# Optimization experiments

Measured on AMD Instinct MI355X. Metric: run time of the kernel, lower is better.

## Reference

```python
import jax, jax.numpy as jnp
import numpy as np

GRID_SIZE = 5
SPLINE_ORDER = 3
GRID_LO, GRID_HI = -1.0, 1.0


def _make_grid():
    # extended knot vector: grid_size + 2*spline_order intervals
    h = (GRID_HI - GRID_LO) / GRID_SIZE
    return jnp.arange(-SPLINE_ORDER, GRID_SIZE + SPLINE_ORDER + 1, dtype=jnp.float32) * h + GRID_LO


def _b_splines(x, grid):
    # x: [N, F] -> bases [N, F, GRID_SIZE + SPLINE_ORDER] via Cox-de Boor recursion
    xg = x[..., None]
    bases = ((xg >= grid[:-1]) & (xg < grid[1:])).astype(x.dtype)
    for k in range(1, SPLINE_ORDER + 1):
        left = (xg - grid[: -(k + 1)]) / (grid[k:-1] - grid[: -(k + 1)])
        right = (grid[k + 1:] - xg) / (grid[k + 1:] - grid[1:-k])
        bases = left * bases[..., :-1] + right * bases[..., 1:]
    return bases


def _kan_linear(x, base_w, spline_w, spline_scaler, grid):
    # x: [N, in], base_w: [out, in], spline_w: [out, in, K], spline_scaler: [out, in]
    base_out = jax.nn.relu(x) @ base_w.T
    n = x.shape[0]
    sw = (spline_w * spline_scaler[..., None]).reshape(base_w.shape[0], -1)  # [out, in*K]
    spline_out = _b_splines(x, grid).reshape(n, -1) @ sw.T
    return base_out + spline_out


def _kan_conv(x, base_w, spline_w, spline_scaler, grid, k=5):
    # x: [B, C, H, W] -> KANLinear over unfolded 5x5 patches (stride 1, VALID)
    B, C, H, W = x.shape
    patches = jax.lax.conv_general_dilated_patches(x, (k, k), (1, 1), 'VALID')  # [B, C*k*k, Ho, Wo]
    Ho, Wo = patches.shape[2], patches.shape[3]
    p = patches.transpose(0, 2, 3, 1).reshape(B * Ho * Wo, C * k * k)
    out = _kan_linear(p, base_w, spline_w, spline_scaler, grid)
    return out.reshape(B, Ho, Wo, -1).transpose(0, 3, 1, 2)


def _avgpool2(x):
    B, C, H, W = x.shape
    return x.reshape(B, C, H // 2, 2, W // 2, 2).mean(axis=(3, 5))


def setup_inputs() -> dict:
    key = jax.random.key(0)
    ks = jax.random.split(key, 13)
    s = 0.1
    return {
        'x': jax.random.normal(ks[0], (1024, 1, 28, 28), jnp.float32),
        'c1_base_w': jax.random.normal(ks[1], (6, 25), jnp.float32) * s,
        'c1_spline_w': jax.random.normal(ks[2], (6, 25, 8), jnp.float32) * s,
        'c1_spline_scaler': jax.random.normal(ks[3], (6, 25), jnp.float32) * s,
        'c2_base_w': jax.random.normal(ks[4], (16, 150), jnp.float32) * s,
        'c2_spline_w': jax.random.normal(ks[5], (16, 150, 8), jnp.float32) * s,
        'c2_spline_scaler': jax.random.normal(ks[6], (16, 150), jnp.float32) * s,
        'fc1_w': jax.random.normal(ks[7], (120, 256), jnp.float32) * s,
        'fc1_b': jax.random.normal(ks[8], (120,), jnp.float32) * s,
        'fc2_w': jax.random.normal(ks[9], (84, 120), jnp.float32) * s,
        'fc2_b': jax.random.normal(ks[10], (84,), jnp.float32) * s,
        'fc3_w': jax.random.normal(ks[11], (62, 84), jnp.float32) * s,
        'fc3_b': jax.random.normal(ks[12], (62,), jnp.float32) * s,
    }


def reference(x, c1_base_w, c1_spline_w, c1_spline_scaler,
              c2_base_w, c2_spline_w, c2_spline_scaler,
              fc1_w, fc1_b, fc2_w, fc2_b, fc3_w, fc3_b):
    grid = _make_grid()
    h = _kan_conv(x, c1_base_w, c1_spline_w, c1_spline_scaler, grid)   # [B,6,24,24]
    h = _avgpool2(h)                                                    # [B,6,12,12]
    h = _kan_conv(h, c2_base_w, c2_spline_w, c2_spline_scaler, grid)   # [B,16,8,8]
    h = _avgpool2(h)                                                    # [B,16,4,4]
    h = h.reshape(h.shape[0], -1)                                       # [B,256]
    h = jax.nn.relu(h @ fc1_w.T + fc1_b)
    h = jax.nn.relu(h @ fc2_w.T + fc2_b)
    return h @ fc3_w.T + fc3_b                                          # [B,62]
```

## Files before the change

### kernel.cpp

```cpp
#include <hip/hip_runtime.h>


typedef _Float16 f16;
typedef f16 f16x8 __attribute__((ext_vector_type(8)));
typedef float f32x4 __attribute__((ext_vector_type(4)));

#define ONE_SIXTH 0.16666666666666666f

__device__ __forceinline__ void spline9(float v, float* __restrict__ f) {
    float u  = 2.5f * v + 5.5f;
    bool valid = (u >= 0.0f) && (u < 11.0f);
    float fi = floorf(u);
    int   i  = (int)fi;
    float w  = u - fi;
    float omw = 1.0f - w;
    float w2 = w * w, w3 = w2 * w;
    float c0 = omw * omw * omw * ONE_SIXTH;
    float c1 = (3.0f * w3 - 6.0f * w2 + 4.0f) * ONE_SIXTH;
    float c2 = (-3.0f * w3 + 3.0f * w2 + 3.0f * w + 1.0f) * ONE_SIXTH;
    float c3 = w3 * ONE_SIXTH;
    int j0 = i - 3;
#pragma unroll
    for (int j = 0; j < 8; ++j) {
        int d = j - j0;
        float val = (d == 0) ? c0 : (d == 1) ? c1 : (d == 2) ? c2 : (d == 3) ? c3 : 0.0f;
        f[j] = valid ? val : 0.0f;
    }
    f[8] = fmaxf(v, 0.0f);
}

__device__ __forceinline__ void spline_chunks(float v, uint4& u0, uint4& u1) {
    float f[9];
    spline9(v, f);
    union { f16 h[8]; uint4 u; } a, b;
#pragma unroll
    for (int j = 0; j < 8; ++j) a.h[j] = (f16)f[j];
    b.u.x = 0u; b.u.y = 0u; b.u.z = 0u; b.u.w = 0u;
    b.h[0] = (f16)f[8];
    u0 = a.u; u1 = b.u;
}

__global__ __launch_bounds__(256) void k_prep(
    const float* __restrict__ c1_bw, const float* __restrict__ c1_sw,
    const float* __restrict__ c1_sc,
    const float* __restrict__ c2_bw, const float* __restrict__ c2_sw,
    const float* __restrict__ c2_sc,
    f16* __restrict__ W1g, f16* __restrict__ W2g)
{
    int t = blockIdx.x * 256 + threadIdx.x;
    if (t < 9216) {
        int tap = t >> 8, r = t & 255;
        int o = r >> 4, k = r & 15;
        float val = 0.0f;
        if (o < 6 && k < 9) {
            int ey = tap / 6, ex = tap - 6 * ey;
            float s = 0.0f;
            for (int a = 0; a < 2; ++a) {
                for (int b = 0; b < 2; ++b) {
                    int dy = ey - a, dx = ex - b;
                    if (dy >= 0 && dy < 5 && dx >= 0 && dx < 5) {
                        int idx = o * 25 + dy * 5 + dx;
                        s += (k == 8) ? c1_bw[idx] : c1_sw[idx * 8 + k] * c1_sc[idx];
                    }
                }
            }
            val = 0.25f * s;
        }
        W1g[t] = (f16)val;
    }
    if (t < 55296) {
        int c = t / 9216, r = t - c * 9216;
        int tap = r >> 8, rr = r & 255;
        int o = rr >> 4, k = rr & 15;
        float val = 0.0f;
        if (k < 9) {
            int ey = tap / 6, ex = tap - 6 * ey;
            float s = 0.0f;
            for (int a = 0; a < 2; ++a) {
                for (int b = 0; b < 2; ++b) {
                    int dy = ey - a, dx = ex - b;
                    if (dy >= 0 && dy < 5 && dx >= 0 && dx < 5) {
                        int idx = o * 150 + c * 25 + dy * 5 + dx;
                        s += (k == 8) ? c2_bw[idx] : c2_sw[idx * 8 + k] * c2_sc[idx];
                    }
                }
            }
            val = 0.25f * s;
        }
        W2g[t] = (f16)val;
    }
}

__global__ __launch_bounds__(192, 3) void k_conv12(
    const float* __restrict__ x, const f16* __restrict__ W1g,
    const f16* __restrict__ W2g, float* __restrict__ h2)
{
    __shared__ uint4  feat[1728];
    __shared__ float  h1l[864];
    __shared__ float4 rbuf[2][64];

    const int img = blockIdx.x;
    const int tid = threadIdx.x;
    const int lane = tid & 63, wv = tid >> 6;
    const int ln15 = lane & 15, g = lane >> 4;
    const int gh = g & 1, gt = g >> 1;

    for (int e = tid; e < 784; e += 192) {
        uint4 u0, u1;
        spline_chunks(x[img * 784 + e], u0, u1);
        int ch = e * 2;
        int q = (ch >> 3) & 7;
        feat[ch ^ q] = u0;
        feat[(ch + 1) ^ q] = u1;
    }
    __syncthreads();

    {
        int ebase[3];
#pragma unroll
        for (int t = 0; t < 3; ++t) {
            int p = (wv * 3 + t) * 16 + ln15;
            int py = p / 12, px = p - py * 12;
            ebase[t] = py * 56 + px * 2;
        }
        const f16* bptr = W1g + (gt * 16 + ln15) * 16 + gh * 8;
        f16x8 bfrag = *(const f16x8*)bptr;
        f32x4 acc[3] = {{0,0,0,0},{0,0,0,0},{0,0,0,0}};

        for (int kc = 0; kc < 18; ++kc) {
            int tap = kc * 2 + gt;
            int ey = (tap * 171) >> 10, ex = tap - ey * 6;
            int eoff = ey * 28 + ex;
            f16x8 bcur = bfrag;
            bptr += 512;
            bfrag = *(const f16x8*)bptr;
#pragma unroll
            for (int t = 0; t < 3; ++t) {
                int ch = (ebase[t] + eoff) * 2 + gh;
                ch ^= (ch >> 3) & 7;
                f16x8 afrag = *(const f16x8*)(&feat[ch]);
                acc[t] = __builtin_amdgcn_mfma_f32_16x16x32_f16(afrag, bcur, acc[t], 0, 0, 0);
            }
        }
        if (ln15 < 6) {
#pragma unroll
            for (int t = 0; t < 3; ++t) {
                int p0 = (wv * 3 + t) * 16 + g * 4;
                *(float4*)&h1l[ln15 * 144 + p0] =
                    make_float4(acc[t][0], acc[t][1], acc[t][2], acc[t][3]);
            }
        }
    }
    __syncthreads();

    for (int e = tid; e < 864; e += 192) {
        uint4 u0, u1;
        spline_chunks(h1l[e], u0, u1);
        int ch = e * 2;
        int q = (ch >> 3) & 7;
        feat[ch ^ q] = u0;
        feat[(ch + 1) ^ q] = u1;
    }
    __syncthreads();

    {
        const int py = ln15 >> 2, px = ln15 & 3;
        const int epx = py * 24 + px * 2;
        const int kk0 = wv * 36;
        const f16* bptr = W2g + ((kk0 * 2 + gt) * 16 + ln15) * 16 + gh * 8;
        f16x8 bfrag = *(const f16x8*)bptr;
        f32x4 acc = {0, 0, 0, 0};

        for (int i = 0; i < 36; ++i) {
            int kk = kk0 + i;
            int c = kk / 18, tk = kk - c * 18;
            int tap = tk * 2 + gt;
            int ey = (tap * 171) >> 10, ex = tap - ey * 6;
            f16x8 bcur = bfrag;
            bptr += 512;
            bfrag = *(const f16x8*)bptr;
            int elem = c * 144 + epx + ey * 12 + ex;
            int ch = elem * 2 + gh;
            ch ^= (ch >> 3) & 7;
            f16x8 afrag = *(const f16x8*)(&feat[ch]);
            acc = __builtin_amdgcn_mfma_f32_16x16x32_f16(afrag, bcur, acc, 0, 0, 0);
        }

        if (wv) rbuf[wv - 1][lane] = make_float4(acc[0], acc[1], acc[2], acc[3]);
        __syncthreads();
        if (wv == 0) {
            float4 r0 = rbuf[0][lane], r1 = rbuf[1][lane];
            *(float4*)&h2[img * 256 + ln15 * 16 + g * 4] =
                make_float4(acc[0] + r0.x + r1.x, acc[1] + r0.y + r1.y,
                            acc[2] + r0.z + r1.z, acc[3] + r0.w + r1.w);
        }
    }
}

__global__ __launch_bounds__(256) void k_fc(
    const float* __restrict__ h2,
    const float* __restrict__ w1, const float* __restrict__ b1,
    const float* __restrict__ w2, const float* __restrict__ b2,
    const float* __restrict__ w3, const float* __restrict__ b3,
    float* __restrict__ out)
{
    __shared__ float xin[8][260];
    __shared__ float a1[8][120];
    __shared__ float a2[8][84];
    const int tid = threadIdx.x;
    const int r0 = blockIdx.x * 8;

    for (int i = tid; i < 2048; i += 256)
        xin[i >> 8][i & 255] = h2[r0 * 256 + i];
    __syncthreads();

    for (int idx = tid; idx < 960; idx += 256) {
        const int o = idx >> 3, r = idx & 7;
        const float* w = w1 + o * 256;
        float s = 0.0f;
#pragma unroll 8
        for (int k = 0; k < 64; ++k) {
            float4 wv = ((const float4*)w)[k];
            float4 xv = *(const float4*)(&xin[r][k * 4]);
            s += wv.x * xv.x + wv.y * xv.y + wv.z * xv.z + wv.w * xv.w;
        }
        a1[r][o] = fmaxf(s + b1[o], 0.0f);
    }
    __syncthreads();

    for (int idx = tid; idx < 672; idx += 256) {
        const int o = idx >> 3, r = idx & 7;
        const float* w = w2 + o * 120;
        float s = 0.0f;
#pragma unroll
        for (int k = 0; k < 30; ++k) {
            float4 wv = ((const float4*)w)[k];
            float4 xv = *(const float4*)(&a1[r][k * 4]);
            s += wv.x * xv.x + wv.y * xv.y + wv.z * xv.z + wv.w * xv.w;
        }
        a2[r][o] = fmaxf(s + b2[o], 0.0f);
    }
    __syncthreads();

    for (int idx = tid; idx < 496; idx += 256) {
        const int o = idx >> 3, r = idx & 7;
        const float* w = w3 + o * 84;
        float s = 0.0f;
#pragma unroll
        for (int k = 0; k < 21; ++k) {
            float4 wv = ((const float4*)w)[k];
            float4 xv = *(const float4*)(&a2[r][k * 4]);
            s += wv.x * xv.x + wv.y * xv.y + wv.z * xv.z + wv.w * xv.w;
        }
        out[(r0 + r) * 62 + o] = s + b3[o];
    }
}

extern "C" void kernel_launch(void* const* d_in, const int* in_sizes, int n_in,
                              void* d_out, int out_size, void* d_ws, size_t ws_size,
                              hipStream_t stream)
{
    (void)in_sizes; (void)n_in; (void)out_size; (void)ws_size;
    const float* x      = (const float*)d_in[0];
    const float* c1_bw  = (const float*)d_in[1];
    const float* c1_sw  = (const float*)d_in[2];
    const float* c1_sc  = (const float*)d_in[3];
    const float* c2_bw  = (const float*)d_in[4];
    const float* c2_sw  = (const float*)d_in[5];
    const float* c2_sc  = (const float*)d_in[6];
    const float* fc1_w  = (const float*)d_in[7];
    const float* fc1_b  = (const float*)d_in[8];
    const float* fc2_w  = (const float*)d_in[9];
    const float* fc2_b  = (const float*)d_in[10];
    const float* fc3_w  = (const float*)d_in[11];
    const float* fc3_b  = (const float*)d_in[12];
    float* out = (float*)d_out;

    char* wsb = (char*)d_ws;
    f16*   W1g = (f16*)(wsb);
    f16*   W2g = (f16*)(wsb + 18432);
    float* h2  = (float*)(wsb + 131072);

    hipLaunchKernelGGL(k_prep, dim3(256), dim3(256), 0, stream,
                       c1_bw, c1_sw, c1_sc, c2_bw, c2_sw, c2_sc, W1g, W2g);
    hipLaunchKernelGGL(k_conv12, dim3(1024), dim3(192), 0, stream,
                       x, W1g, W2g, h2);
    hipLaunchKernelGGL(k_fc, dim3(128), dim3(256), 0, stream,
                       h2, fc1_w, fc1_b, fc2_w, fc2_b, fc3_w, fc3_b, out);
}
```

Baseline: 45.57 us.

## Fuse FC layers into conv kernel, process two images per block

Merges the conv kernel and the FC-stack kernel into one launch. Each 384-thread block handles two images, and conv2 results stay in shared memory instead of going through a global h2 buffer. The conv2 MFMA loop now alternates between two accumulators to shorten the dependency chain. This removes a kernel launch and a global round-trip. In exchange, the FC weights are now re-read per pair of images rather than per eight, and FC utilisation per block is lower, so more time goes to the serial FC tail.

```diff
diff --git a/kernel.cpp b/kernel.cpp
--- a/kernel.cpp
+++ b/kernel.cpp
@@ -91,27 +91,37 @@
     }
 }
 
-__global__ __launch_bounds__(192, 3) void k_conv12(
+__global__ __launch_bounds__(384, 2) void k_fused(
     const float* __restrict__ x, const f16* __restrict__ W1g,
-    const f16* __restrict__ W2g, float* __restrict__ h2)
+    const f16* __restrict__ W2g,
+    const float* __restrict__ w1, const float* __restrict__ b1,
+    const float* __restrict__ w2, const float* __restrict__ b2,
+    const float* __restrict__ w3, const float* __restrict__ b3,
+    float* __restrict__ out)
 {
-    __shared__ uint4  feat[1728];
-    __shared__ float  h1l[864];
-    __shared__ float4 rbuf[2][64];
-
-    const int img = blockIdx.x;
+    __shared__ __align__(16) uint4  feat[2][1728];
+    __shared__ __align__(16) float  h1l[2][864];
+    __shared__ __align__(16) float4 rbuf[2][2][64];
+    __shared__ __align__(16) float  h2l[2][256];
+    __shared__ __align__(16) float  a1[2][120];
+    __shared__ __align__(16) float  a2[2][84];
+
+    const int i0 = blockIdx.x * 2;
     const int tid = threadIdx.x;
     const int lane = tid & 63, wv = tid >> 6;
+    const int im = wv >= 3 ? 1 : 0;
+    const int wvv = wv - 3 * im;
     const int ln15 = lane & 15, g = lane >> 4;
     const int gh = g & 1, gt = g >> 1;
 
-    for (int e = tid; e < 784; e += 192) {
+    for (int e = tid; e < 1568; e += 384) {
+        int m = e >= 784, r = e - 784 * m;
         uint4 u0, u1;
-        spline_chunks(x[img * 784 + e], u0, u1);
-        int ch = e * 2;
+        spline_chunks(x[(i0 + m) * 784 + r], u0, u1);
+        int ch = r * 2;
         int q = (ch >> 3) & 7;
-        feat[ch ^ q] = u0;
-        feat[(ch + 1) ^ q] = u1;
+        feat[m][ch ^ q] = u0;
+        feat[m][(ch + 1) ^ q] = u1;
     }
     __syncthreads();
 
@@ -119,7 +129,7 @@
         int ebase[3];
 #pragma unroll
         for (int t = 0; t < 3; ++t) {
-            int p = (wv * 3 + t) * 16 + ln15;
+            int p = (wvv * 3 + t) * 16 + ln15;
             int py = p / 12, px = p - py * 12;
             ebase[t] = py * 56 + px * 2;
         }
@@ -138,121 +148,112 @@
             for (int t = 0; t < 3; ++t) {
                 int ch = (ebase[t] + eoff) * 2 + gh;
                 ch ^= (ch >> 3) & 7;
-                f16x8 afrag = *(const f16x8*)(&feat[ch]);
+                f16x8 afrag = *(const f16x8*)(&feat[im][ch]);
                 acc[t] = __builtin_amdgcn_mfma_f32_16x16x32_f16(afrag, bcur, acc[t], 0, 0, 0);
             }
         }
         if (ln15 < 6) {
 #pragma unroll
             for (int t = 0; t < 3; ++t) {
-                int p0 = (wv * 3 + t) * 16 + g * 4;
-                *(float4*)&h1l[ln15 * 144 + p0] =
+                int p0 = (wvv * 3 + t) * 16 + g * 4;
+                *(float4*)&h1l[im][ln15 * 144 + p0] =
                     make_float4(acc[t][0], acc[t][1], acc[t][2], acc[t][3]);
             }
         }
     }
     __syncthreads();
 
-    for (int e = tid; e < 864; e += 192) {
+    for (int e = tid; e < 1728; e += 384) {
+        int m = e >= 864, r = e - 864 * m;
         uint4 u0, u1;
-        spline_chunks(h1l[e], u0, u1);
-        int ch = e * 2;
+        spline_chunks(h1l[m][r], u0, u1);
+        int ch = r * 2;
         int q = (ch >> 3) & 7;
-        feat[ch ^ q] = u0;
-        feat[(ch + 1) ^ q] = u1;
+        feat[m][ch ^ q] = u0;
+        feat[m][(ch + 1) ^ q] = u1;
     }
     __syncthreads();
 
     {
         const int py = ln15 >> 2, px = ln15 & 3;
         const int epx = py * 24 + px * 2;
-        const int kk0 = wv * 36;
+        const int kk0 = wvv * 36;
         const f16* bptr = W2g + ((kk0 * 2 + gt) * 16 + ln15) * 16 + gh * 8;
         f16x8 bfrag = *(const f16x8*)bptr;
-        f32x4 acc = {0, 0, 0, 0};
-
-        for (int i = 0; i < 36; ++i) {
-            int kk = kk0 + i;
-            int c = kk / 18, tk = kk - c * 18;
-            int tap = tk * 2 + gt;
-            int ey = (tap * 171) >> 10, ex = tap - ey * 6;
-            f16x8 bcur = bfrag;
-            bptr += 512;
-            bfrag = *(const f16x8*)bptr;
-            int elem = c * 144 + epx + ey * 12 + ex;
-            int ch = elem * 2 + gh;
-            ch ^= (ch >> 3) & 7;
-            f16x8 afrag = *(const f16x8*)(&feat[ch]);
-            acc = __builtin_amdgcn_mfma_f32_16x16x32_f16(afrag, bcur, acc, 0, 0, 0);
-        }
-
-        if (wv) rbuf[wv - 1][lane] = make_float4(acc[0], acc[1], acc[2], acc[3]);
+        f32x4 accA = {0, 0, 0, 0}, accB = {0, 0, 0, 0};
+
+        for (int i = 0; i < 36; i += 2) {
+#pragma unroll
+            for (int s = 0; s < 2; ++s) {
+                int kk = kk0 + i + s;
+                int c = kk / 18, tk = kk - c * 18;
+                int tap = tk * 2 + gt;
+                int ey = (tap * 171) >> 10, ex = tap - ey * 6;
+                f16x8 bcur = bfrag;
+                bptr += 512;
+                bfrag = *(const f16x8*)bptr;
+                int elem = c * 144 + epx + ey * 12 + ex;
+                int ch = elem * 2 + gh;
+                ch ^= (ch >> 3) & 7;
+                f16x8 afrag = *(const f16x8*)(&feat[im][ch]);
+                if (s == 0)
+                    accA = __builtin_amdgcn_mfma_f32_16x16x32_f16(afrag, bcur, accA, 0, 0, 0);
+                else
+                    accB = __builtin_amdgcn_mfma_f32_16x16x32_f16(afrag, bcur, accB, 0, 0, 0);
+            }
+        }
+        f32x4 acc = accA + accB;
+
+        if (wvv) rbuf[im][wvv - 1][lane] = make_float4(acc[0], acc[1], acc[2], acc[3]);
         __syncthreads();
-        if (wv == 0) {
-            float4 r0 = rbuf[0][lane], r1 = rbuf[1][lane];
-            *(float4*)&h2[img * 256 + ln15 * 16 + g * 4] =
+        if (wvv == 0) {
+            float4 r0 = rbuf[im][0][lane], r1 = rbuf[im][1][lane];
+            *(float4*)&h2l[im][ln15 * 16 + g * 4] =
                 make_float4(acc[0] + r0.x + r1.x, acc[1] + r0.y + r1.y,
                             acc[2] + r0.z + r1.z, acc[3] + r0.w + r1.w);
         }
     }
-}
-
-__global__ __launch_bounds__(256) void k_fc(
-    const float* __restrict__ h2,
-    const float* __restrict__ w1, const float* __restrict__ b1,
-    const float* __restrict__ w2, const float* __restrict__ b2,
-    const float* __restrict__ w3, const float* __restrict__ b3,
-    float* __restrict__ out)
-{
-    __shared__ float xin[8][260];
-    __shared__ float a1[8][120];
-    __shared__ float a2[8][84];
-    const int tid = threadIdx.x;
-    const int r0 = blockIdx.x * 8;
-
-    for (int i = tid; i < 2048; i += 256)
-        xin[i >> 8][i & 255] = h2[r0 * 256 + i];
-    __syncthreads();
-
-    for (int idx = tid; idx < 960; idx += 256) {
-        const int o = idx >> 3, r = idx & 7;
+    __syncthreads();
+
+    if (tid < 240) {
+        const int m = tid >= 120, o = tid - 120 * m;
         const float* w = w1 + o * 256;
         float s = 0.0f;
 #pragma unroll 8
         for (int k = 0; k < 64; ++k) {
-            float4 wv = ((const float4*)w)[k];
-            float4 xv = *(const float4*)(&xin[r][k * 4]);
-            s += wv.x * xv.x + wv.y * xv.y + wv.z * xv.z + wv.w * xv.w;
-        }
-        a1[r][o] = fmaxf(s + b1[o], 0.0f);
-    }
-    __syncthreads();
-
-    for (int idx = tid; idx < 672; idx += 256) {
-        const int o = idx >> 3, r = idx & 7;
+            float4 wv4 = ((const float4*)w)[k];
+            float4 xv = *(const float4*)(&h2l[m][k * 4]);
+            s += wv4.x * xv.x + wv4.y * xv.y + wv4.z * xv.z + wv4.w * xv.w;
+        }
+        a1[m][o] = fmaxf(s + b1[o], 0.0f);
+    }
+    __syncthreads();
+
+    if (tid < 168) {
+        const int m = tid >= 84, o = tid - 84 * m;
         const float* w = w2 + o * 120;
         float s = 0.0f;
 #pragma unroll
         for (int k = 0; k < 30; ++k) {
-            float4 wv = ((const float4*)w)[k];
-            float4 xv = *(const float4*)(&a1[r][k * 4]);
-            s += wv.x * xv.x + wv.y * xv.y + wv.z * xv.z + wv.w * xv.w;
-        }
-        a2[r][o] = fmaxf(s + b2[o], 0.0f);
-    }
-    __syncthreads();
-
-    for (int idx = tid; idx < 496; idx += 256) {
-        const int o = idx >> 3, r = idx & 7;
+            float4 wv4 = ((const float4*)w)[k];
+            float4 xv = *(const float4*)(&a1[m][k * 4]);
+            s += wv4.x * xv.x + wv4.y * xv.y + wv4.z * xv.z + wv4.w * xv.w;
+        }
+        a2[m][o] = fmaxf(s + b2[o], 0.0f);
+    }
+    __syncthreads();
+
+    if (tid < 124) {
+        const int m = tid >= 62, o = tid - 62 * m;
         const float* w = w3 + o * 84;
         float s = 0.0f;
 #pragma unroll
         for (int k = 0; k < 21; ++k) {
-            float4 wv = ((const float4*)w)[k];
-            float4 xv = *(const float4*)(&a2[r][k * 4]);
-            s += wv.x * xv.x + wv.y * xv.y + wv.z * xv.z + wv.w * xv.w;
-        }
-        out[(r0 + r) * 62 + o] = s + b3[o];
+            float4 wv4 = ((const float4*)w)[k];
+            float4 xv = *(const float4*)(&a2[m][k * 4]);
+            s += wv4.x * xv.x + wv4.y * xv.y + wv4.z * xv.z + wv4.w * xv.w;
+        }
+        out[(i0 + m) * 62 + o] = s + b3[o];
     }
 }
 
@@ -277,14 +278,12 @@
     float* out = (float*)d_out;
 
     char* wsb = (char*)d_ws;
-    f16*   W1g = (f16*)(wsb);
-    f16*   W2g = (f16*)(wsb + 18432);
-    float* h2  = (float*)(wsb + 131072);
+    f16* W1g = (f16*)(wsb);
+    f16* W2g = (f16*)(wsb + 18432);
 
     hipLaunchKernelGGL(k_prep, dim3(256), dim3(256), 0, stream,
                        c1_bw, c1_sw, c1_sc, c2_bw, c2_sw, c2_sc, W1g, W2g);
-    hipLaunchKernelGGL(k_conv12, dim3(1024), dim3(192), 0, stream,
-                       x, W1g, W2g, h2);
-    hipLaunchKernelGGL(k_fc, dim3(128), dim3(256), 0, stream,
-                       h2, fc1_w, fc1_b, fc2_w, fc2_b, fc3_w, fc3_b, out);
-}
+    hipLaunchKernelGGL(k_fused, dim3(512), dim3(384), 0, stream,
+                       x, W1g, W2g,
+                       fc1_w, fc1_b, fc2_w, fc2_b, fc3_w, fc3_b, out);
+}
```

Measured after the change: 60.04 us. 31.7% more time.
